# Optimization experiments

Measured on AMD Instinct MI355X. Metric: run time of the kernel, lower is better.

The kernel has to match this reference:

```python
import jax, jax.numpy as jnp
import numpy as np

N, N_SPINS, N_HIDDEN = 8192, 1024, 1024


def setup_inputs() -> dict:
    key = jax.random.key(0)
    ks = jax.random.split(key, 6)
    s_in = 1.0 / np.sqrt(N_SPINS)
    s_h = 1.0 / np.sqrt(N_HIDDEN)
    return {
        "x": jax.random.normal(ks[0], (N, N_SPINS), dtype=jnp.float32),
        "W_in": jax.random.normal(ks[1], (N_HIDDEN, N_SPINS), dtype=jnp.float32) * s_in,
        "b_in": jax.random.normal(ks[2], (N_HIDDEN,), dtype=jnp.float32) * s_in,
        "Wq": jax.random.normal(ks[3], (N_HIDDEN, N_HIDDEN), dtype=jnp.float32) * s_h,
        "Wk": jax.random.normal(ks[4], (N_HIDDEN, N_HIDDEN), dtype=jnp.float32) * s_h,
        "Wv": jax.random.normal(ks[5], (N_HIDDEN, N_HIDDEN), dtype=jnp.float32) * s_h,
    }


def reference(x, W_in, b_in, Wq, Wk, Wv):
    # embedding: Linear(n_spins, n_hidden)  -> h: [N, H]
    h = x @ W_in.T + b_in
    q = h @ Wq.T                      # [N, H]
    k = h @ Wk.T                      # [N, H]
    v = h @ Wv.T                      # [N, H]
    scores = (q @ k.T) * 0.25         # [N, N], scale 1/4 as in source
    attn = jax.nn.softmax(scores, axis=0)  # softmax over dim=0 (columns)
    out = attn @ v                    # [N, H]
    # log(cosh(z)) = |z| + log1p(exp(-2|z|)) - log(2), numerically stable
    a = jnp.abs(out)
    logcosh = a + jnp.log1p(jnp.exp(-2.0 * a)) - jnp.log(jnp.asarray(2.0, out.dtype))
    return jnp.sum(logcosh, axis=-1)  # [N]
```

## Files before the change

kernel.cpp:

```cpp
#include <hip/hip_runtime.h>
#include <hip/hip_bf16.h>
#include <cstdint>
#include <cstddef>

#define NTOK 8192
#define NHID 1024

typedef __attribute__((ext_vector_type(8))) __bf16 bf16x8;
typedef __attribute__((ext_vector_type(4))) float f32x4;

__device__ __forceinline__ unsigned short f2bf(float f) {
    union { float f; unsigned u; } v; v.f = f;
    unsigned r = v.u + 0x7FFF + ((v.u >> 16) & 1);
    return (unsigned short)(r >> 16);
}

__device__ __forceinline__ float bf2f(unsigned short u) {
    union { unsigned u; float f; } v; v.u = ((unsigned)u) << 16;
    return v.f;
}

__device__ __forceinline__ void async_copy16(const void* gsrc, void* ldsdst) {
    __builtin_amdgcn_global_load_lds(
        (const __attribute__((address_space(1))) unsigned int*)gsrc,
        (__attribute__((address_space(3))) unsigned int*)ldsdst,
        16, 0, 0);
}

template <int EPI, bool SWAP>
__global__ __launch_bounds__(512, 2) void gemm_bt4(
    const unsigned short* __restrict__ A,
    const unsigned short* __restrict__ B,
    void* __restrict__ C,
    const float* __restrict__ bias,
    float* __restrict__ zsum,
    float scale, int M, int N, int K, int lda, int ldb)
{
    __shared__ __attribute__((aligned(16))) unsigned short lds[3][24576];

    const int tid  = threadIdx.x;
    const int wave = tid >> 6;
    const int lane = tid & 63;
    const int bm = (SWAP ? blockIdx.x : blockIdx.y) * 256;
    const int bn = (SWAP ? blockIdx.y : blockIdx.x) * 128;
    const size_t ldaz = (size_t)lda;
    const size_t ldbz = (size_t)ldb;

    const int srow = lane >> 3;
    const int scol = ((lane & 7) ^ srow) * 8;
    const unsigned short* Ag[4];
    const unsigned short* Bg[2];
    int Aoff[4], Boff[2];
#pragma unroll
    for (int t = 0; t < 4; ++t) {
        int r = (wave * 4 + t) * 8 + srow;
        Ag[t] = A + (size_t)(bm + r) * ldaz + scol;
        Aoff[t] = (wave * 4 + t) * 512;
    }
#pragma unroll
    for (int t = 0; t < 2; ++t) {
        int r = (wave * 2 + t) * 8 + srow;
        Bg[t] = B + (size_t)(bn + r) * ldbz + scol;
        Boff[t] = 16384 + (wave * 2 + t) * 512;
    }

    const int wm = (wave >> 1) * 64;
    const int wn = (wave & 1) * 64;
    const int fr = lane & 15;
    const int frl = fr & 7;
    const int q = lane >> 4;

    const int pc0 = (q ^ frl) * 8;
    const int pc1 = ((4 + q) ^ frl) * 8;

    f32x4 acc[4][4] = {};

    const int nt = K >> 6;

    {
        unsigned short* b0 = &lds[0][0];
        unsigned short* b1 = &lds[1][0];
#pragma unroll
        for (int u = 0; u < 4; ++u) { async_copy16(Ag[u], b0 + Aoff[u]); Ag[u] += 64; }
#pragma unroll
        for (int u = 0; u < 2; ++u) { async_copy16(Bg[u], b0 + Boff[u]); Bg[u] += 64; }
#pragma unroll
        for (int u = 0; u < 4; ++u) { async_copy16(Ag[u], b1 + Aoff[u]); Ag[u] += 64; }
#pragma unroll
        for (int u = 0; u < 2; ++u) { async_copy16(Bg[u], b1 + Boff[u]); Bg[u] += 64; }
        asm volatile("s_waitcnt vmcnt(6)" ::: "memory");
        asm volatile("s_barrier" ::: "memory");
    }

    bf16x8 a0_0, a0_1, a0_2, a0_3, b0_0, b0_1, b0_2, b0_3;
    bf16x8 a1_0, a1_1, a1_2, a1_3, b1_0, b1_1, b1_2, b1_3;

    {
        const unsigned short* As = &lds[0][0];
        const unsigned short* Bs = &lds[0][16384];
        a0_0 = *(const bf16x8*)&As[(wm +  0 + fr) * 64 + pc0];
        a0_1 = *(const bf16x8*)&As[(wm + 16 + fr) * 64 + pc0];
        a0_2 = *(const bf16x8*)&As[(wm + 32 + fr) * 64 + pc0];
        a0_3 = *(const bf16x8*)&As[(wm + 48 + fr) * 64 + pc0];
        b0_0 = *(const bf16x8*)&Bs[(wn +  0 + fr) * 64 + pc0];
        b0_1 = *(const bf16x8*)&Bs[(wn + 16 + fr) * 64 + pc0];
        b0_2 = *(const bf16x8*)&Bs[(wn + 32 + fr) * 64 + pc0];
        b0_3 = *(const bf16x8*)&Bs[(wn + 48 + fr) * 64 + pc0];
    }

#define MFMA16(AA0, AA1, AA2, AA3, BB0, BB1, BB2, BB3)                         \
    do {                                                                       \
        __builtin_amdgcn_s_setprio(1);                                         \
        acc[0][0] = __builtin_amdgcn_mfma_f32_16x16x32_bf16(AA0, BB0, acc[0][0], 0, 0, 0); \
        acc[0][1] = __builtin_amdgcn_mfma_f32_16x16x32_bf16(AA0, BB1, acc[0][1], 0, 0, 0); \
        acc[0][2] = __builtin_amdgcn_mfma_f32_16x16x32_bf16(AA0, BB2, acc[0][2], 0, 0, 0); \
        acc[0][3] = __builtin_amdgcn_mfma_f32_16x16x32_bf16(AA0, BB3, acc[0][3], 0, 0, 0); \
        acc[1][0] = __builtin_amdgcn_mfma_f32_16x16x32_bf16(AA1, BB0, acc[1][0], 0, 0, 0); \
        acc[1][1] = __builtin_amdgcn_mfma_f32_16x16x32_bf16(AA1, BB1, acc[1][1], 0, 0, 0); \
        acc[1][2] = __builtin_amdgcn_mfma_f32_16x16x32_bf16(AA1, BB2, acc[1][2], 0, 0, 0); \
        acc[1][3] = __builtin_amdgcn_mfma_f32_16x16x32_bf16(AA1, BB3, acc[1][3], 0, 0, 0); \
        acc[2][0] = __builtin_amdgcn_mfma_f32_16x16x32_bf16(AA2, BB0, acc[2][0], 0, 0, 0); \
        acc[2][1] = __builtin_amdgcn_mfma_f32_16x16x32_bf16(AA2, BB1, acc[2][1], 0, 0, 0); \
        acc[2][2] = __builtin_amdgcn_mfma_f32_16x16x32_bf16(AA2, BB2, acc[2][2], 0, 0, 0); \
        acc[2][3] = __builtin_amdgcn_mfma_f32_16x16x32_bf16(AA2, BB3, acc[2][3], 0, 0, 0); \
        acc[3][0] = __builtin_amdgcn_mfma_f32_16x16x32_bf16(AA3, BB0, acc[3][0], 0, 0, 0); \
        acc[3][1] = __builtin_amdgcn_mfma_f32_16x16x32_bf16(AA3, BB1, acc[3][1], 0, 0, 0); \
        acc[3][2] = __builtin_amdgcn_mfma_f32_16x16x32_bf16(AA3, BB2, acc[3][2], 0, 0, 0); \
        acc[3][3] = __builtin_amdgcn_mfma_f32_16x16x32_bf16(AA3, BB3, acc[3][3], 0, 0, 0); \
        __builtin_amdgcn_s_setprio(0);                                         \
    } while (0)

    int cb = 0;
    int sb = 2;
    for (int t = 0; t < nt; ++t) {
        const bool pf = (t + 2 < nt);
        const unsigned short* As = &lds[cb][0];
        const unsigned short* Bs = &lds[cb][16384];
        unsigned short* Sb = &lds[sb][0];
        const int nb = (cb == 2) ? 0 : cb + 1;
        const unsigned short* An = &lds[nb][0];
        const unsigned short* Bn = &lds[nb][16384];

        a1_0 = *(const bf16x8*)&As[(wm +  0 + fr) * 64 + pc1];
        a1_1 = *(const bf16x8*)&As[(wm + 16 + fr) * 64 + pc1];
        a1_2 = *(const bf16x8*)&As[(wm + 32 + fr) * 64 + pc1];
        a1_3 = *(const bf16x8*)&As[(wm + 48 + fr) * 64 + pc1];
        b1_0 = *(const bf16x8*)&Bs[(wn +  0 + fr) * 64 + pc1];
        b1_1 = *(const bf16x8*)&Bs[(wn + 16 + fr) * 64 + pc1];
        b1_2 = *(const bf16x8*)&Bs[(wn + 32 + fr) * 64 + pc1];
        b1_3 = *(const bf16x8*)&Bs[(wn + 48 + fr) * 64 + pc1];
        if (pf) {
#pragma unroll
            for (int u = 0; u < 4; ++u) { async_copy16(Ag[u], Sb + Aoff[u]); Ag[u] += 64; }
        }
        __builtin_amdgcn_sched_barrier(0);
        MFMA16(a0_0, a0_1, a0_2, a0_3, b0_0, b0_1, b0_2, b0_3);
        if (t < nt - 2) asm volatile("s_waitcnt vmcnt(4)" ::: "memory");
        else            asm volatile("s_waitcnt vmcnt(0)" ::: "memory");
        asm volatile("s_barrier" ::: "memory");

        if (t + 1 < nt) {
            a0_0 = *(const bf16x8*)&An[(wm +  0 + fr) * 64 + pc0];
            a0_1 = *(const bf16x8*)&An[(wm + 16 + fr) * 64 + pc0];
            a0_2 = *(const bf16x8*)&An[(wm + 32 + fr) * 64 + pc0];
            a0_3 = *(const bf16x8*)&An[(wm + 48 + fr) * 64 + pc0];
            b0_0 = *(const bf16x8*)&Bn[(wn +  0 + fr) * 64 + pc0];
            b0_1 = *(const bf16x8*)&Bn[(wn + 16 + fr) * 64 + pc0];
            b0_2 = *(const bf16x8*)&Bn[(wn + 32 + fr) * 64 + pc0];
            b0_3 = *(const bf16x8*)&Bn[(wn + 48 + fr) * 64 + pc0];
        }
        if (pf) {
#pragma unroll
            for (int u = 0; u < 2; ++u) { async_copy16(Bg[u], Sb + Boff[u]); Bg[u] += 64; }
        }
        __builtin_amdgcn_sched_barrier(0);
        MFMA16(a1_0, a1_1, a1_2, a1_3, b1_0, b1_1, b1_2, b1_3);
        asm volatile("s_barrier" ::: "memory");

        if (pf) sb = (sb == 2) ? 0 : sb + 1;
        cb = nb;
    }
#undef MFMA16

    const int erow = q * 4;
#pragma unroll
    for (int j = 0; j < 4; ++j) {
        const int gcol = bn + wn + j * 16 + fr;
        const float bv = (EPI == 1 && bias) ? bias[gcol] : 0.0f;
        float colsum = 0.0f;
#pragma unroll
        for (int i = 0; i < 4; ++i) {
            const int grow0 = bm + wm + i * 16 + erow;
#pragma unroll
            for (int r = 0; r < 4; ++r) {
                float v;
                if (EPI == 2) {
                    v = __expf(fmaf(acc[i][j][r], scale, -64.0f));
                    colsum += v;
                } else {
                    v = acc[i][j][r] * scale + bv;
                }
                size_t idx = (size_t)(grow0 + r) * N + gcol;
                if (EPI == 0) ((float*)C)[idx] = v;
                else          ((unsigned short*)C)[idx] = f2bf(v);
            }
        }
        if (EPI == 2) {
            colsum += __shfl_xor(colsum, 16, 64);
            colsum += __shfl_xor(colsum, 32, 64);
            if (q == 0) atomicAdd(&zsum[gcol], colsum);
        }
    }
}

__global__ void cvt_all(const float4* __restrict__ x,
                        const float4* __restrict__ w0,
                        const float4* __restrict__ w1,
                        const float4* __restrict__ w2,
                        const float4* __restrict__ w3,
                        ushort4* __restrict__ xb,
                        ushort4* __restrict__ wdst,
                        float4* __restrict__ pz4,
                        int n4x, int n4w)
{
    int i = blockIdx.x * blockDim.x + threadIdx.x;
    int n4 = n4x + 4 * n4w;
    if (i >= n4) {
        int zi = i - n4;
        if (zi < 2048) pz4[zi] = make_float4(0.f, 0.f, 0.f, 0.f);
        return;
    }
    float4 f;
    ushort4* dst;
    if (i < n4x) {
        f = x[i]; dst = xb + i;
    } else {
        int r = i - n4x;
        int seg = r / n4w, off = r % n4w;
        const float4* src = (seg == 0) ? w0 : (seg == 1) ? w1 : (seg == 2) ? w2 : w3;
        f = src[off]; dst = wdst + r;
    }
    ushort4 o;
    o.x = f2bf(f.x); o.y = f2bf(f.y); o.z = f2bf(f.z); o.w = f2bf(f.w);
    *dst = o;
}

__global__ __launch_bounds__(256) void transpose_scale(
    const unsigned short* __restrict__ v,
    const float* __restrict__ z,
    unsigned short* __restrict__ vt)
{
    __shared__ float lds[64 * 65];
    const int tid = threadIdx.x;
    const int j0 = blockIdx.x * 64;
    const int h0 = blockIdx.y * 64;
    const int c = tid & 63;
    const int r0 = tid >> 6;
#pragma unroll
    for (int it = 0; it < 16; ++it) {
        int r = it * 4 + r0;
        lds[r * 65 + c] = bf2f(v[(size_t)(j0 + r) * 3072 + h0 + c]);
    }
    __syncthreads();
    const float rz = 1.0f / z[j0 + c];
#pragma unroll
    for (int it = 0; it < 16; ++it) {
        int r = it * 4 + r0;
        vt[(size_t)(h0 + r) * NTOK + j0 + c] = f2bf(lds[c * 65 + r] * rz);
    }
}

__global__ void logcosh_rowsum(const ushort4* __restrict__ O4,
                               float* __restrict__ out)
{
    const float LN2 = 0.69314718055994531f;
    int row = blockIdx.x;
    ushort4 u = O4[(size_t)row * 256 + threadIdx.x];
    float s = 0.0f, a;
    a = fabsf(bf2f(u.x)); s += a + log1pf(__expf(-2.0f * a));
    a = fabsf(bf2f(u.y)); s += a + log1pf(__expf(-2.0f * a));
    a = fabsf(bf2f(u.z)); s += a + log1pf(__expf(-2.0f * a));
    a = fabsf(bf2f(u.w)); s += a + log1pf(__expf(-2.0f * a));
    s -= 4.0f * LN2;
    for (int off = 32; off; off >>= 1) s += __shfl_down(s, off, 64);
    __shared__ float red[4];
    if ((threadIdx.x & 63) == 0) red[threadIdx.x >> 6] = s;
    __syncthreads();
    if (threadIdx.x == 0) out[row] = red[0] + red[1] + red[2] + red[3];
}

extern "C" void kernel_launch(void* const* d_in, const int* in_sizes, int n_in,
                              void* d_out, int out_size, void* d_ws, size_t ws_size,
                              hipStream_t stream)
{
    (void)in_sizes; (void)n_in; (void)out_size; (void)ws_size;

    const float* x    = (const float*)d_in[0];
    const float* W_in = (const float*)d_in[1];
    const float* b_in = (const float*)d_in[2];
    const float* Wq   = (const float*)d_in[3];
    const float* Wk   = (const float*)d_in[4];
    const float* Wv   = (const float*)d_in[5];
    float* out = (float*)d_out;

    char* w = (char*)d_ws;
    const size_t MiB = 1024 * 1024;
    unsigned short* Pb     = (unsigned short*)(w);
    unsigned short* qkv    = (unsigned short*)(w + 128 * MiB);
    unsigned short* xb     = (unsigned short*)(w + 128 * MiB);
    unsigned short* outb   = (unsigned short*)(w + 128 * MiB);
    unsigned short* hb     = (unsigned short*)(w + 176 * MiB);
    unsigned short* vtb    = (unsigned short*)(w + 176 * MiB);
    unsigned short* wib    = (unsigned short*)(w + 192 * MiB);
    unsigned short* wqkvb  = (unsigned short*)(w + 194 * MiB);
    float*          pz     = (float*)         (w + 200 * MiB);

    {
        int n4x = NTOK * NHID / 4;
        int n4w = NHID * NHID / 4;
        int n4  = n4x + 4 * n4w;
        cvt_all<<<n4 / 256 + 8, 256, 0, stream>>>(
            (const float4*)x, (const float4*)W_in, (const float4*)Wq,
            (const float4*)Wk, (const float4*)Wv,
            (ushort4*)xb, (ushort4*)wib, (float4*)pz, n4x, n4w);
    }

    dim3 gNH(NHID / 128, NTOK / 256);
    gemm_bt4<1, false><<<gNH, 512, 0, stream>>>(
        xb, wib, hb, b_in, nullptr, 1.0f, NTOK, NHID, NHID, NHID, NHID);

    dim3 gQKV(3 * NHID / 128, NTOK / 256);
    gemm_bt4<1, false><<<gQKV, 512, 0, stream>>>(
        hb, wqkvb, qkv, nullptr, nullptr, 1.0f, NTOK, 3 * NHID, NHID, NHID, NHID);

    dim3 gS(NTOK / 128, NTOK / 256);
    gemm_bt4<2, false><<<gS, 512, 0, stream>>>(
        qkv, qkv + NHID, Pb, nullptr, pz, 0.25f, NTOK, NTOK, NHID,
        3 * NHID, 3 * NHID);

    dim3 gT(NTOK / 64, NHID / 64);
    transpose_scale<<<gT, 256, 0, stream>>>(qkv + 2 * NHID, pz, vtb);

    dim3 gO(NTOK / 256, NHID / 128);
    gemm_bt4<1, true><<<gO, 512, 0, stream>>>(
        Pb, vtb, outb, nullptr, nullptr, 1.0f, NTOK, NHID, NTOK, NTOK, NTOK);

    logcosh_rowsum<<<NTOK, 256, 0, stream>>>((const ushort4*)outb, out);
}
```

Before: 474.1 us.

## Use 256x256 square-tile GEMM kernel for the QK^T scores stage

Adds a new GEMM kernel with 256x256 output tiles, 2-stage LDS double buffering and split A/B staging, and uses it for the large 8192x8192 scores GEMM with the exp/column-sum epilogue. Larger square tiles raise arithmetic intensity and halve the global reloads of A per output. The cost is 128 accumulator registers per lane and 128KB of LDS, which may lower occupancy and latency hiding, and the shallower pipeline may expose load latency.

```diff
diff --git a/kernel.cpp b/kernel.cpp
--- a/kernel.cpp
+++ b/kernel.cpp
@@ -25,6 +25,148 @@
         (const __attribute__((address_space(1))) unsigned int*)gsrc,
         (__attribute__((address_space(3))) unsigned int*)ldsdst,
         16, 0, 0);
+}
+
+template <int EPI, bool SWAP>
+__global__ __launch_bounds__(512, 2) void gemm_sq(
+    const unsigned short* __restrict__ A,
+    const unsigned short* __restrict__ B,
+    void* __restrict__ C,
+    const float* __restrict__ bias,
+    float* __restrict__ zsum,
+    float scale, int M, int N, int K, int lda, int ldb)
+{
+    __shared__ __attribute__((aligned(16))) unsigned short lds[2][32768];
+
+    const int tid  = threadIdx.x;
+    const int wave = tid >> 6;
+    const int lane = tid & 63;
+    const int bm = (SWAP ? blockIdx.x : blockIdx.y) * 256;
+    const int bn = (SWAP ? blockIdx.y : blockIdx.x) * 256;
+    const size_t ldaz = (size_t)lda;
+    const size_t ldbz = (size_t)ldb;
+
+    const int srow = lane >> 3;
+    const int scol = ((lane & 7) ^ srow) * 8;
+    const unsigned short* Ag[4];
+    const unsigned short* Bg[4];
+    int off[4];
+#pragma unroll
+    for (int t = 0; t < 4; ++t) {
+        int r = (wave * 4 + t) * 8 + srow;
+        Ag[t] = A + (size_t)(bm + r) * ldaz + scol;
+        Bg[t] = B + (size_t)(bn + r) * ldbz + scol;
+        off[t] = (wave * 4 + t) * 512;
+    }
+
+    const int wm = (wave >> 2) * 128;
+    const int wn = (wave & 3) * 64;
+    const int fr = lane & 15;
+    const int frl = fr & 7;
+    const int q = lane >> 4;
+
+    const int pc0 = (q ^ frl) * 8;
+    const int pc1 = ((4 + q) ^ frl) * 8;
+
+    f32x4 acc[8][4] = {};
+
+    const int nt = K >> 6;
+
+    auto stageA = [&](int s) {
+#pragma unroll
+        for (int t = 0; t < 4; ++t) { async_copy16(Ag[t], &lds[s][off[t]]); Ag[t] += 64; }
+    };
+    auto stageB = [&](int s) {
+#pragma unroll
+        for (int t = 0; t < 4; ++t) { async_copy16(Bg[t], &lds[s][16384 + off[t]]); Bg[t] += 64; }
+    };
+
+    stageA(0);
+    stageB(0);
+    stageA(1);
+    asm volatile("s_waitcnt vmcnt(4)" ::: "memory");
+    asm volatile("s_barrier" ::: "memory");
+
+    for (int t = 0; t < nt; ++t) {
+        const int cb = t & 1;
+        const unsigned short* As = &lds[cb][0];
+        const unsigned short* Bs = &lds[cb][16384];
+
+        if (t + 1 < nt) stageB(cb ^ 1);
+
+        {
+            bf16x8 a[8], b[4];
+#pragma unroll
+            for (int i = 0; i < 8; ++i)
+                a[i] = *(const bf16x8*)&As[(wm + i * 16 + fr) * 64 + pc0];
+#pragma unroll
+            for (int j = 0; j < 4; ++j)
+                b[j] = *(const bf16x8*)&Bs[(wn + j * 16 + fr) * 64 + pc0];
+            __builtin_amdgcn_s_setprio(1);
+#pragma unroll
+            for (int i = 0; i < 8; ++i)
+#pragma unroll
+                for (int j = 0; j < 4; ++j)
+                    acc[i][j] = __builtin_amdgcn_mfma_f32_16x16x32_bf16(
+                        a[i], b[j], acc[i][j], 0, 0, 0);
+            __builtin_amdgcn_s_setprio(0);
+        }
+        {
+            bf16x8 a[8], b[4];
+#pragma unroll
+            for (int i = 0; i < 8; ++i)
+                a[i] = *(const bf16x8*)&As[(wm + i * 16 + fr) * 64 + pc1];
+#pragma unroll
+            for (int j = 0; j < 4; ++j)
+                b[j] = *(const bf16x8*)&Bs[(wn + j * 16 + fr) * 64 + pc1];
+            __builtin_amdgcn_s_setprio(1);
+#pragma unroll
+            for (int i = 0; i < 8; ++i)
+#pragma unroll
+                for (int j = 0; j < 4; ++j)
+                    acc[i][j] = __builtin_amdgcn_mfma_f32_16x16x32_bf16(
+                        a[i], b[j], acc[i][j], 0, 0, 0);
+            __builtin_amdgcn_s_setprio(0);
+        }
+
+        if (t + 1 < nt) {
+            asm volatile("s_barrier" ::: "memory");
+            if (t + 2 < nt) stageA(cb);
+            if (t < nt - 2) asm volatile("s_waitcnt vmcnt(4)" ::: "memory");
+            else            asm volatile("s_waitcnt vmcnt(0)" ::: "memory");
+            asm volatile("s_barrier" ::: "memory");
+        }
+    }
+
+    const int erow = q * 4;
+#pragma unroll
+    for (int j = 0; j < 4; ++j) {
+        const int gcol = bn + wn + j * 16 + fr;
+        const float bv = (EPI == 1 && bias) ? bias[gcol] : 0.0f;
+        float colsum = 0.0f;
+#pragma unroll
+        for (int i = 0; i < 8; ++i) {
+            const int grow0 = bm + wm + i * 16 + erow;
+#pragma unroll
+            for (int r = 0; r < 4; ++r) {
+                float v;
+                if (EPI == 2) {
+                    v = __expf(fmaf(acc[i][j][r], scale, -64.0f));
+                    colsum += v;
+                } else {
+                    v = acc[i][j][r] * scale + bv;
+                }
+                size_t idx = (size_t)(grow0 + r) * N + gcol;
+                if (EPI == 0) ((float*)C)[idx] = v;
+                else          ((unsigned short*)C)[idx] = f2bf(v);
+            }
+        }
+        if (EPI == 2) {
+            colsum += __shfl_xor(colsum, 16, 64);
+            colsum += __shfl_xor(colsum, 32, 64);
+            if (q == 0) atomicAdd(&zsum[gcol], colsum);
+        }
+    }
 }
 
 template <int EPI, bool SWAP>
@@ -333,8 +475,8 @@
     gemm_bt4<1, false><<<gQKV, 512, 0, stream>>>(
         hb, wqkvb, qkv, nullptr, nullptr, 1.0f, NTOK, 3 * NHID, NHID, NHID, NHID);
 
-    dim3 gS(NTOK / 128, NTOK / 256);
-    gemm_bt4<2, false><<<gS, 512, 0, stream>>>(
+    dim3 gS(NTOK / 256, NTOK / 256);
+    gemm_sq<2, false><<<gS, 512, 0, stream>>>(
         qkv, qkv + NHID, Pb, nullptr, pz, 0.25f, NTOK, NTOK, NHID,
         3 * NHID, 3 * NHID);
 
```

Result: no change. 474.6 us (+0.1%).
